# Kernel tuning notes

Hardware: AMD Instinct MI355X
Metric: run time of the kernel (lower is better)

The kernel has to match this reference:

```python
import jax, jax.numpy as jnp
import numpy as np

H = 32  # hidden size fixed by the module


def setup_inputs() -> dict:
    key = jax.random.key(0)
    ks = jax.random.split(key, 7)
    B, T, D = 1024, 512, 64
    s_ih = 1.0 / np.sqrt(H)
    return {
        "x": jax.random.normal(ks[0], (B, T, D), dtype=jnp.float32),
        "W_ih": jax.random.normal(ks[1], (3 * H, D), dtype=jnp.float32) * s_ih,
        "W_hh": jax.random.normal(ks[2], (3 * H, H), dtype=jnp.float32) * s_ih,
        "b_ih": jax.random.normal(ks[3], (3 * H,), dtype=jnp.float32) * s_ih,
        "b_hh": jax.random.normal(ks[4], (3 * H,), dtype=jnp.float32) * s_ih,
        "W_fc": jax.random.normal(ks[5], (1, H), dtype=jnp.float32) * s_ih,
        "b_fc": jax.random.normal(ks[6], (1,), dtype=jnp.float32) * s_ih,
    }


def _gru_last_hidden(x, W_ih, W_hh, b_ih, b_hh):
    # Precompute input-side gates for all timesteps in one big GEMM: [B,T,3H]
    xg = jnp.einsum("btd,gd->btg", x, W_ih) + b_ih
    xg = jnp.swapaxes(xg, 0, 1)  # [T,B,3H] for scan
    B = x.shape[0]
    h0 = jnp.zeros((B, H), dtype=x.dtype)

    def step(h, xg_t):
        gh = h @ W_hh.T + b_hh  # [B,3H]
        xr, xz, xn = xg_t[:, :H], xg_t[:, H:2 * H], xg_t[:, 2 * H:]
        hr, hz, hn = gh[:, :H], gh[:, H:2 * H], gh[:, 2 * H:]
        r = jax.nn.sigmoid(xr + hr)
        z = jax.nn.sigmoid(xz + hz)
        n = jnp.tanh(xn + r * hn)
        h_new = (1.0 - z) * n + z * h
        return h_new, None

    h_last, _ = jax.lax.scan(step, h0, xg)
    return h_last  # [B,H]


def reference(x, W_ih, W_hh, b_ih, b_hh, W_fc, b_fc):
    # GRU -> dropout (eval mode: identity) -> Linear on last timestep
    h_last = _gru_last_hidden(x, W_ih, W_hh, b_ih, b_hh)
    return h_last @ W_fc.T + b_fc  # [B,1]
```

## Files before the change

kernel.cpp:

```cpp
#include <hip/hip_runtime.h>

#define TS 512
#define DD 64
#define HH 32

typedef _Float16 half2v __attribute__((ext_vector_type(2)));

__device__ __forceinline__ float fdot2(half2v a, half2v b, float c) {
#if __has_builtin(__builtin_amdgcn_fdot2)
    return __builtin_amdgcn_fdot2(a, b, c, false);
#else
    return fmaf((float)a[0], (float)b[0], fmaf((float)a[1], (float)b[1], c));
#endif
}

__device__ __forceinline__ float fast_sigmoid(float a) {
    return __builtin_amdgcn_rcpf(1.0f + __expf(-a));
}

__global__ __launch_bounds__(64, 1) void gru_fused(
    const float* __restrict__ x,
    const float* __restrict__ Wih,
    const float* __restrict__ Whh,
    const float* __restrict__ bih,
    const float* __restrict__ bhh,
    const float* __restrict__ Wfc,
    const float* __restrict__ bfc,
    float* __restrict__ out)
{
    __shared__ __align__(16) _Float16 xs16[4][DD];
    __shared__ __align__(16) _Float16 hs16[HH];

    const int b    = blockIdx.x;
    const int lane = threadIdx.x;
    const int s    = lane >> 5;
    const int h    = lane & 31;

    half2v wr2[16], wz2[16], wn2[16];
    {
        const float4* pr = reinterpret_cast<const float4*>(Wih + (0 * HH + h) * DD + s * 32);
        const float4* pz = reinterpret_cast<const float4*>(Wih + (1 * HH + h) * DD + s * 32);
        const float4* pn = reinterpret_cast<const float4*>(Wih + (2 * HH + h) * DD + s * 32);
#pragma unroll
        for (int k = 0; k < 8; ++k) {
            float4 a = pr[k];
            wr2[2*k]   = half2v{(_Float16)a.x, (_Float16)a.y};
            wr2[2*k+1] = half2v{(_Float16)a.z, (_Float16)a.w};
            float4 c = pz[k];
            wz2[2*k]   = half2v{(_Float16)c.x, (_Float16)c.y};
            wz2[2*k+1] = half2v{(_Float16)c.z, (_Float16)c.w};
            float4 e = pn[k];
            wn2[2*k]   = half2v{(_Float16)e.x, (_Float16)e.y};
            wn2[2*k+1] = half2v{(_Float16)e.z, (_Float16)e.w};
        }
    }
    half2v ur2[8], uz2[8], un2[8];
    {
        const float4* pr = reinterpret_cast<const float4*>(Whh + (0 * HH + h) * HH + s * 16);
        const float4* pz = reinterpret_cast<const float4*>(Whh + (1 * HH + h) * HH + s * 16);
        const float4* pn = reinterpret_cast<const float4*>(Whh + (2 * HH + h) * HH + s * 16);
#pragma unroll
        for (int k = 0; k < 4; ++k) {
            float4 a = pr[k];
            ur2[2*k]   = half2v{(_Float16)a.x, (_Float16)a.y};
            ur2[2*k+1] = half2v{(_Float16)a.z, (_Float16)a.w};
            float4 c = pz[k];
            uz2[2*k]   = half2v{(_Float16)c.x, (_Float16)c.y};
            uz2[2*k+1] = half2v{(_Float16)c.z, (_Float16)c.w};
            float4 e = pn[k];
            un2[2*k]   = half2v{(_Float16)e.x, (_Float16)e.y};
            un2[2*k+1] = half2v{(_Float16)e.z, (_Float16)e.w};
        }
    }

    const float br  = bih[h]          + bhh[h];
    const float bz  = bih[HH + h]     + bhh[HH + h];
    const float bxn = bih[2 * HH + h];
    const float bhn = bhh[2 * HH + h];
    const float wfc = Wfc[h];
    const float bf0 = bfc[0];

    const float* xrow = x + (size_t)b * TS * DD;

    float p0 = xrow[0 * DD + lane];
    float p1 = xrow[1 * DD + lane];
    float p2 = xrow[2 * DD + lane];
    float ra = xrow[3 * DD + lane];
    float rb = xrow[4 * DD + lane];
    float rc = xrow[5 * DD + lane];
    xs16[0][lane] = (_Float16)p0;
    xs16[1][lane] = (_Float16)p1;
    xs16[2][lane] = (_Float16)p2;
    __builtin_amdgcn_wave_barrier();

    float h_own = 0.0f;
    half2v hv2[8];
#pragma unroll
    for (int k = 0; k < 8; ++k) hv2[k] = half2v{(_Float16)0.0f, (_Float16)0.0f};

    float ar, az, an;
    {
        const uint4* xp = reinterpret_cast<const uint4*>(&xs16[0][s * 32]);
        ar = 0.f; az = 0.f; an = 0.f;
#pragma unroll
        for (int k = 0; k < 4; ++k) {
            uint4 q = xp[k];
            half2v v0 = __builtin_bit_cast(half2v, q.x);
            half2v v1 = __builtin_bit_cast(half2v, q.y);
            half2v v2 = __builtin_bit_cast(half2v, q.z);
            half2v v3 = __builtin_bit_cast(half2v, q.w);
            ar = fdot2(wr2[4*k  ], v0, ar);
            az = fdot2(wz2[4*k  ], v0, az);
            an = fdot2(wn2[4*k  ], v0, an);
            ar = fdot2(wr2[4*k+1], v1, ar);
            az = fdot2(wz2[4*k+1], v1, az);
            an = fdot2(wn2[4*k+1], v1, an);
            ar = fdot2(wr2[4*k+2], v2, ar);
            az = fdot2(wz2[4*k+2], v2, az);
            an = fdot2(wn2[4*k+2], v2, an);
            ar = fdot2(wr2[4*k+3], v3, ar);
            az = fdot2(wz2[4*k+3], v3, az);
            an = fdot2(wn2[4*k+3], v3, an);
        }
    }

    for (int t = 0; t < TS; ++t) {
        xs16[(t + 3) & 3][lane] = (_Float16)ra;
        ra = rb; rb = rc;
        int tf = t + 6; if (tf > TS - 1) tf = TS - 1;
        rc = xrow[tf * DD + lane];

        float gr = 0.f, gz = 0.f, gn = 0.f;
#pragma unroll
        for (int k = 0; k < 8; ++k) {
            gr = fdot2(ur2[k], hv2[k], gr);
            gz = fdot2(uz2[k], hv2[k], gz);
            gn = fdot2(un2[k], hv2[k], gn);
        }

        float tr = ar + gr;  tr += __shfl_xor(tr, 32);
        float tz = az + gz;  tz += __shfl_xor(tz, 32);
        float txn = an + __shfl_xor(an, 32);
        float tgn = gn + __shfl_xor(gn, 32);

        float r = fast_sigmoid(tr + br);
        float z = fast_sigmoid(tz + bz);
        float npre = txn + bxn + r * (tgn + bhn);
        npre = fminf(fmaxf(npre, -30.f), 30.f);
        float e2 = __expf(-2.f * npre);
        float n = (1.f - e2) * __builtin_amdgcn_rcpf(1.f + e2);
        h_own = n + z * (h_own - n);

        hs16[h] = (_Float16)h_own;
        __builtin_amdgcn_wave_barrier();
        {
            const uint4* hp = reinterpret_cast<const uint4*>(&hs16[s * 16]);
            uint4 q0 = hp[0];
            uint4 q1 = hp[1];
            hv2[0] = __builtin_bit_cast(half2v, q0.x);
            hv2[1] = __builtin_bit_cast(half2v, q0.y);
            hv2[2] = __builtin_bit_cast(half2v, q0.z);
            hv2[3] = __builtin_bit_cast(half2v, q0.w);
            hv2[4] = __builtin_bit_cast(half2v, q1.x);
            hv2[5] = __builtin_bit_cast(half2v, q1.y);
            hv2[6] = __builtin_bit_cast(half2v, q1.z);
            hv2[7] = __builtin_bit_cast(half2v, q1.w);
        }

        if (t + 1 < TS) {
            const uint4* xp = reinterpret_cast<const uint4*>(&xs16[(t + 1) & 3][s * 32]);
            ar = 0.f; az = 0.f; an = 0.f;
#pragma unroll
            for (int k = 0; k < 4; ++k) {
                uint4 q = xp[k];
                half2v v0 = __builtin_bit_cast(half2v, q.x);
                half2v v1 = __builtin_bit_cast(half2v, q.y);
                half2v v2 = __builtin_bit_cast(half2v, q.z);
                half2v v3 = __builtin_bit_cast(half2v, q.w);
                ar = fdot2(wr2[4*k  ], v0, ar);
                az = fdot2(wz2[4*k  ], v0, az);
                an = fdot2(wn2[4*k  ], v0, an);
                ar = fdot2(wr2[4*k+1], v1, ar);
                az = fdot2(wz2[4*k+1], v1, az);
                an = fdot2(wn2[4*k+1], v1, an);
                ar = fdot2(wr2[4*k+2], v2, ar);
                az = fdot2(wz2[4*k+2], v2, az);
                an = fdot2(wn2[4*k+2], v2, an);
                ar = fdot2(wr2[4*k+3], v3, ar);
                az = fdot2(wz2[4*k+3], v3, az);
                an = fdot2(wn2[4*k+3], v3, an);
            }
        }
    }

    float v = h_own * wfc;
#pragma unroll
    for (int off = 32; off >= 1; off >>= 1) v += __shfl_xor(v, off);
    if (lane == 0) out[b] = 0.5f * v + bf0;
}

extern "C" void kernel_launch(void* const* d_in, const int* in_sizes, int n_in,
                              void* d_out, int out_size, void* d_ws, size_t ws_size,
                              hipStream_t stream) {
    const float* x    = (const float*)d_in[0];
    const float* Wih  = (const float*)d_in[1];
    const float* Whh  = (const float*)d_in[2];
    const float* bih  = (const float*)d_in[3];
    const float* bhh  = (const float*)d_in[4];
    const float* Wfc  = (const float*)d_in[5];
    const float* bfc  = (const float*)d_in[6];
    float* out = (float*)d_out;

    const int B = in_sizes[0] / (TS * DD);
    gru_fused<<<dim3(B), dim3(64), 0, stream>>>(x, Wih, Whh, bih, bhh, Wfc, bfc, out);
}
```

Baseline: 190.5 us.

## Split input projection into separate kernel writing fp16 gates to workspace

The input-side gate projection moves out of the serial recurrence into its own kernel. That kernel uses three waves per batch row and writes biased fp16 gate pre-activations to the workspace. The recurrence kernel then only prefetches those gates and runs the hidden-state dot products, split across two accumulators, which shortens the per-step dependency chain. The cost is an extra write and read of a large fp16 intermediate plus a second launch. A fallback to the original fused kernel is kept for when the workspace is too small.

```diff
diff --git a/kernel.cpp b/kernel.cpp
--- a/kernel.cpp
+++ b/kernel.cpp
@@ -3,6 +3,7 @@
 #define TS 512
 #define DD 64
 #define HH 32
+#define NG 96
 
 typedef _Float16 half2v __attribute__((ext_vector_type(2)));
 
@@ -18,17 +19,78 @@
     return __builtin_amdgcn_rcpf(1.0f + __expf(-a));
 }
 
-__global__ __launch_bounds__(64, 1) void gru_fused(
+__global__ __launch_bounds__(192, 1) void xg_gemm(
     const float* __restrict__ x,
     const float* __restrict__ Wih,
+    const float* __restrict__ bih,
+    _Float16* __restrict__ xg)
+{
+    __shared__ __align__(16) _Float16 xsw[3][4][DD];
+
+    const int b    = blockIdx.x;
+    const int tid  = threadIdx.x;
+    const int w    = tid >> 6;
+    const int lane = tid & 63;
+    const int j    = lane >> 5;
+    const int g    = w * 32 + (lane & 31);
+
+    half2v wg[16];
+    {
+        const float4* pw = reinterpret_cast<const float4*>(Wih + g * DD + j * 32);
+#pragma unroll
+        for (int k = 0; k < 8; ++k) {
+            float4 a = pw[k];
+            wg[2*k]   = half2v{(_Float16)a.x, (_Float16)a.y};
+            wg[2*k+1] = half2v{(_Float16)a.z, (_Float16)a.w};
+        }
+    }
+    const float bg = bih[g];
+
+    const float* xr = x + (size_t)b * TS * DD;
+    _Float16* og = xg + (size_t)b * TS * NG;
+
+    float q0 = xr[0*DD + lane];
+    float q1 = xr[1*DD + lane];
+    float q2 = xr[2*DD + lane];
+    float ra = xr[3*DD + lane];
+    float rb = xr[4*DD + lane];
+    float rc = xr[5*DD + lane];
+    xsw[w][0][lane] = (_Float16)q0;
+    xsw[w][1][lane] = (_Float16)q1;
+    xsw[w][2][lane] = (_Float16)q2;
+    __builtin_amdgcn_wave_barrier();
+
+    for (int t = 0; t < TS; ++t) {
+        xsw[w][(t + 3) & 3][lane] = (_Float16)ra;
+        ra = rb; rb = rc;
+        int tf = t + 6; if (tf > TS - 1) tf = TS - 1;
+        rc = xr[tf * DD + lane];
+        __builtin_amdgcn_wave_barrier();
+
+        const uint4* xp = reinterpret_cast<const uint4*>(&xsw[w][t & 3][j * 32]);
+        float a0 = 0.f, a1 = 0.f;
+#pragma unroll
+        for (int k = 0; k < 4; ++k) {
+            uint4 q = xp[k];
+            a0 = fdot2(wg[4*k  ], __builtin_bit_cast(half2v, q.x), a0);
+            a1 = fdot2(wg[4*k+1], __builtin_bit_cast(half2v, q.y), a1);
+            a0 = fdot2(wg[4*k+2], __builtin_bit_cast(half2v, q.z), a0);
+            a1 = fdot2(wg[4*k+3], __builtin_bit_cast(half2v, q.w), a1);
+        }
+        float acc = a0 + a1;
+        acc += __shfl_xor(acc, 32);
+        if (j == 0) og[t * NG + g] = (_Float16)(acc + bg);
+    }
+}
+
+__global__ __launch_bounds__(64, 1) void gru_rec(
+    const _Float16* __restrict__ xg,
     const float* __restrict__ Whh,
-    const float* __restrict__ bih,
     const float* __restrict__ bhh,
     const float* __restrict__ Wfc,
     const float* __restrict__ bfc,
     float* __restrict__ out)
 {
-    __shared__ __align__(16) _Float16 xs16[4][DD];
     __shared__ __align__(16) _Float16 hs16[HH];
 
     const int b    = blockIdx.x;
@@ -36,29 +98,11 @@
     const int s    = lane >> 5;
     const int h    = lane & 31;
 
-    half2v wr2[16], wz2[16], wn2[16];
-    {
-        const float4* pr = reinterpret_cast<const float4*>(Wih + (0 * HH + h) * DD + s * 32);
-        const float4* pz = reinterpret_cast<const float4*>(Wih + (1 * HH + h) * DD + s * 32);
-        const float4* pn = reinterpret_cast<const float4*>(Wih + (2 * HH + h) * DD + s * 32);
-#pragma unroll
-        for (int k = 0; k < 8; ++k) {
-            float4 a = pr[k];
-            wr2[2*k]   = half2v{(_Float16)a.x, (_Float16)a.y};
-            wr2[2*k+1] = half2v{(_Float16)a.z, (_Float16)a.w};
-            float4 c = pz[k];
-            wz2[2*k]   = half2v{(_Float16)c.x, (_Float16)c.y};
-            wz2[2*k+1] = half2v{(_Float16)c.z, (_Float16)c.w};
-            float4 e = pn[k];
-            wn2[2*k]   = half2v{(_Float16)e.x, (_Float16)e.y};
-            wn2[2*k+1] = half2v{(_Float16)e.z, (_Float16)e.w};
-        }
-    }
     half2v ur2[8], uz2[8], un2[8];
     {
-        const float4* pr = reinterpret_cast<const float4*>(Whh + (0 * HH + h) * HH + s * 16);
-        const float4* pz = reinterpret_cast<const float4*>(Whh + (1 * HH + h) * HH + s * 16);
-        const float4* pn = reinterpret_cast<const float4*>(Whh + (2 * HH + h) * HH + s * 16);
+        const float4* pr = reinterpret_cast<const float4*>(Whh + (0*HH + h)*HH + s*16);
+        const float4* pz = reinterpret_cast<const float4*>(Whh + (1*HH + h)*HH + s*16);
+        const float4* pn = reinterpret_cast<const float4*>(Whh + (2*HH + h)*HH + s*16);
 #pragma unroll
         for (int k = 0; k < 4; ++k) {
             float4 a = pr[k];
@@ -73,79 +117,55 @@
         }
     }
 
-    const float br  = bih[h]          + bhh[h];
-    const float bz  = bih[HH + h]     + bhh[HH + h];
-    const float bxn = bih[2 * HH + h];
-    const float bhn = bhh[2 * HH + h];
+    const float cr  = bhh[h];
+    const float cz  = bhh[HH + h];
+    const float cn  = bhh[2*HH + h];
     const float wfc = Wfc[h];
     const float bf0 = bfc[0];
 
-    const float* xrow = x + (size_t)b * TS * DD;
-
-    float p0 = xrow[0 * DD + lane];
-    float p1 = xrow[1 * DD + lane];
-    float p2 = xrow[2 * DD + lane];
-    float ra = xrow[3 * DD + lane];
-    float rb = xrow[4 * DD + lane];
-    float rc = xrow[5 * DD + lane];
-    xs16[0][lane] = (_Float16)p0;
-    xs16[1][lane] = (_Float16)p1;
-    xs16[2][lane] = (_Float16)p2;
-    __builtin_amdgcn_wave_barrier();
-
-    float h_own = 0.0f;
+    const _Float16* xb = xg + (size_t)b * TS * NG;
+
+    _Float16 xra = xb[0*NG + h],        xrb = xb[1*NG + h],        xrc = xb[2*NG + h];
+    _Float16 xza = xb[0*NG + HH + h],   xzb = xb[1*NG + HH + h],   xzc = xb[2*NG + HH + h];
+    _Float16 xna = xb[0*NG + 2*HH + h], xnb = xb[1*NG + 2*HH + h], xnc = xb[2*NG + 2*HH + h];
+
+    float h_own = 0.f;
     half2v hv2[8];
 #pragma unroll
     for (int k = 0; k < 8; ++k) hv2[k] = half2v{(_Float16)0.0f, (_Float16)0.0f};
 
-    float ar, az, an;
-    {
-        const uint4* xp = reinterpret_cast<const uint4*>(&xs16[0][s * 32]);
-        ar = 0.f; az = 0.f; an = 0.f;
-#pragma unroll
-        for (int k = 0; k < 4; ++k) {
-            uint4 q = xp[k];
-            half2v v0 = __builtin_bit_cast(half2v, q.x);
-            half2v v1 = __builtin_bit_cast(half2v, q.y);
-            half2v v2 = __builtin_bit_cast(half2v, q.z);
-            half2v v3 = __builtin_bit_cast(half2v, q.w);
-            ar = fdot2(wr2[4*k  ], v0, ar);
-            az = fdot2(wz2[4*k  ], v0, az);
-            an = fdot2(wn2[4*k  ], v0, an);
-            ar = fdot2(wr2[4*k+1], v1, ar);
-            az = fdot2(wz2[4*k+1], v1, az);
-            an = fdot2(wn2[4*k+1], v1, an);
-            ar = fdot2(wr2[4*k+2], v2, ar);
-            az = fdot2(wz2[4*k+2], v2, az);
-            an = fdot2(wn2[4*k+2], v2, an);
-            ar = fdot2(wr2[4*k+3], v3, ar);
-            az = fdot2(wz2[4*k+3], v3, az);
-            an = fdot2(wn2[4*k+3], v3, an);
-        }
-    }
-
     for (int t = 0; t < TS; ++t) {
-        xs16[(t + 3) & 3][lane] = (_Float16)ra;
-        ra = rb; rb = rc;
-        int tf = t + 6; if (tf > TS - 1) tf = TS - 1;
-        rc = xrow[tf * DD + lane];
-
-        float gr = 0.f, gz = 0.f, gn = 0.f;
-#pragma unroll
-        for (int k = 0; k < 8; ++k) {
-            gr = fdot2(ur2[k], hv2[k], gr);
-            gz = fdot2(uz2[k], hv2[k], gz);
-            gn = fdot2(un2[k], hv2[k], gn);
-        }
-
-        float tr = ar + gr;  tr += __shfl_xor(tr, 32);
-        float tz = az + gz;  tz += __shfl_xor(tz, 32);
-        float txn = an + __shfl_xor(an, 32);
-        float tgn = gn + __shfl_xor(gn, 32);
-
-        float r = fast_sigmoid(tr + br);
-        float z = fast_sigmoid(tz + bz);
-        float npre = txn + bxn + r * (tgn + bhn);
+        float xrv = (float)xra;
+        float xzv = (float)xza;
+        float xnv = (float)xna;
+        xra = xrb; xrb = xrc;
+        xza = xzb; xzb = xzc;
+        xna = xnb; xnb = xnc;
+        int tf = t + 3; if (tf > TS - 1) tf = TS - 1;
+        xrc = xb[tf*NG + h];
+        xzc = xb[tf*NG + HH + h];
+        xnc = xb[tf*NG + 2*HH + h];
+
+        float gr0 = 0.f, gr1 = 0.f, gz0 = 0.f, gz1 = 0.f, gn0 = 0.f, gn1 = 0.f;
+#pragma unroll
+        for (int k = 0; k < 4; ++k) {
+            gr0 = fdot2(ur2[2*k  ], hv2[2*k  ], gr0);
+            gr1 = fdot2(ur2[2*k+1], hv2[2*k+1], gr1);
+            gz0 = fdot2(uz2[2*k  ], hv2[2*k  ], gz0);
+            gz1 = fdot2(uz2[2*k+1], hv2[2*k+1], gz1);
+            gn0 = fdot2(un2[2*k  ], hv2[2*k  ], gn0);
+            gn1 = fdot2(un2[2*k+1], hv2[2*k+1], gn1);
+        }
+        float gr = gr0 + gr1;
+        float gz = gz0 + gz1;
+        float gn = gn0 + gn1;
+        gr += __shfl_xor(gr, 32);
+        gz += __shfl_xor(gz, 32);
+        gn += __shfl_xor(gn, 32);
+
+        float r = fast_sigmoid(xrv + cr + gr);
+        float z = fast_sigmoid(xzv + cz + gz);
+        float npre = xnv + r * (gn + cn);
         npre = fminf(fmaxf(npre, -30.f), 30.f);
         float e2 = __expf(-2.f * npre);
         float n = (1.f - e2) * __builtin_amdgcn_rcpf(1.f + e2);
@@ -166,6 +186,154 @@
             hv2[6] = __builtin_bit_cast(half2v, q1.z);
             hv2[7] = __builtin_bit_cast(half2v, q1.w);
         }
+    }
+
+    float v = h_own * wfc;
+#pragma unroll
+    for (int off = 32; off >= 1; off >>= 1) v += __shfl_xor(v, off);
+    if (lane == 0) out[b] = 0.5f * v + bf0;
+}
+
+__global__ __launch_bounds__(64, 1) void gru_fused_fb(
+    const float* __restrict__ x,
+    const float* __restrict__ Wih,
+    const float* __restrict__ Whh,
+    const float* __restrict__ bih,
+    const float* __restrict__ bhh,
+    const float* __restrict__ Wfc,
+    const float* __restrict__ bfc,
+    float* __restrict__ out)
+{
+    __shared__ __align__(16) _Float16 xs16[4][DD];
+    __shared__ __align__(16) _Float16 hs16[HH];
+
+    const int b    = blockIdx.x;
+    const int lane = threadIdx.x;
+    const int s    = lane >> 5;
+    const int h    = lane & 31;
+
+    half2v wr2[16], wz2[16], wn2[16];
+    {
+        const float4* pr = reinterpret_cast<const float4*>(Wih + (0*HH + h)*DD + s*32);
+        const float4* pz = reinterpret_cast<const float4*>(Wih + (1*HH + h)*DD + s*32);
+        const float4* pn = reinterpret_cast<const float4*>(Wih + (2*HH + h)*DD + s*32);
+#pragma unroll
+        for (int k = 0; k < 8; ++k) {
+            float4 a = pr[k];
+            wr2[2*k]   = half2v{(_Float16)a.x, (_Float16)a.y};
+            wr2[2*k+1] = half2v{(_Float16)a.z, (_Float16)a.w};
+            float4 c = pz[k];
+            wz2[2*k]   = half2v{(_Float16)c.x, (_Float16)c.y};
+            wz2[2*k+1] = half2v{(_Float16)c.z, (_Float16)c.w};
+            float4 e = pn[k];
+            wn2[2*k]   = half2v{(_Float16)e.x, (_Float16)e.y};
+            wn2[2*k+1] = half2v{(_Float16)e.z, (_Float16)e.w};
+        }
+    }
+    half2v ur2[8], uz2[8], un2[8];
+    {
+        const float4* pr = reinterpret_cast<const float4*>(Whh + (0*HH + h)*HH + s*16);
+        const float4* pz = reinterpret_cast<const float4*>(Whh + (1*HH + h)*HH + s*16);
+        const float4* pn = reinterpret_cast<const float4*>(Whh + (2*HH + h)*HH + s*16);
+#pragma unroll
+        for (int k = 0; k < 4; ++k) {
+            float4 a = pr[k];
+            ur2[2*k]   = half2v{(_Float16)a.x, (_Float16)a.y};
+            ur2[2*k+1] = half2v{(_Float16)a.z, (_Float16)a.w};
+            float4 c = pz[k];
+            uz2[2*k]   = half2v{(_Float16)c.x, (_Float16)c.y};
+            uz2[2*k+1] = half2v{(_Float16)c.z, (_Float16)c.w};
+            float4 e = pn[k];
+            un2[2*k]   = half2v{(_Float16)e.x, (_Float16)e.y};
+            un2[2*k+1] = half2v{(_Float16)e.z, (_Float16)e.w};
+        }
+    }
+
+    const float br  = bih[h]        + bhh[h];
+    const float bz  = bih[HH + h]   + bhh[HH + h];
+    const float bxn = bih[2*HH + h];
+    const float bhn = bhh[2*HH + h];
+    const float wfc = Wfc[h];
+    const float bf0 = bfc[0];
+
+    const float* xrow = x + (size_t)b * TS * DD;
+
+    float p0 = xrow[0*DD + lane];
+    float p1 = xrow[1*DD + lane];
+    float p2 = xrow[2*DD + lane];
+    float ra = xrow[3*DD + lane];
+    float rb = xrow[4*DD + lane];
+    float rc = xrow[5*DD + lane];
+    xs16[0][lane] = (_Float16)p0;
+    xs16[1][lane] = (_Float16)p1;
+    xs16[2][lane] = (_Float16)p2;
+    __builtin_amdgcn_wave_barrier();
+
+    float h_own = 0.0f;
+    half2v hv2[8];
+#pragma unroll
+    for (int k = 0; k < 8; ++k) hv2[k] = half2v{(_Float16)0.0f, (_Float16)0.0f};
+
+    float ar, az, an;
+    {
+        const uint4* xp = reinterpret_cast<const uint4*>(&xs16[0][s * 32]);
+        ar = 0.f; az = 0.f; an = 0.f;
+#pragma unroll
+        for (int k = 0; k < 4; ++k) {
+            uint4 q = xp[k];
+            half2v v0 = __builtin_bit_cast(half2v, q.x);
+            half2v v1 = __builtin_bit_cast(half2v, q.y);
+            half2v v2 = __builtin_bit_cast(half2v, q.z);
+            half2v v3 = __builtin_bit_cast(half2v, q.w);
+            ar = fdot2(wr2[4*k  ], v0, ar);  az = fdot2(wz2[4*k  ], v0, az);  an = fdot2(wn2[4*k  ], v0, an);
+            ar = fdot2(wr2[4*k+1], v1, ar);  az = fdot2(wz2[4*k+1], v1, az);  an = fdot2(wn2[4*k+1], v1, an);
+            ar = fdot2(wr2[4*k+2], v2, ar);  az = fdot2(wz2[4*k+2], v2, az);  an = fdot2(wn2[4*k+2], v2, an);
+            ar = fdot2(wr2[4*k+3], v3, ar);  az = fdot2(wz2[4*k+3], v3, az);  an = fdot2(wn2[4*k+3], v3, an);
+        }
+    }
+
+    for (int t = 0; t < TS; ++t) {
+        xs16[(t + 3) & 3][lane] = (_Float16)ra;
+        ra = rb; rb = rc;
+        int tf = t + 6; if (tf > TS - 1) tf = TS - 1;
+        rc = xrow[tf * DD + lane];
+
+        float gr = 0.f, gz = 0.f, gn = 0.f;
+#pragma unroll
+        for (int k = 0; k < 8; ++k) {
+            gr = fdot2(ur2[k], hv2[k], gr);
+            gz = fdot2(uz2[k], hv2[k], gz);
+            gn = fdot2(un2[k], hv2[k], gn);
+        }
+
+        float tr = ar + gr;  tr += __shfl_xor(tr, 32);
+        float tz = az + gz;  tz += __shfl_xor(tz, 32);
+        float txn = an + __shfl_xor(an, 32);
+        float tgn = gn + __shfl_xor(gn, 32);
+
+        float r = fast_sigmoid(tr + br);
+        float z = fast_sigmoid(tz + bz);
+        float npre = txn + bxn + r * (tgn + bhn);
+        npre = fminf(fmaxf(npre, -30.f), 30.f);
+        float e2 = __expf(-2.f * npre);
+        float n = (1.f - e2) * __builtin_amdgcn_rcpf(1.f + e2);
+        h_own = n + z * (h_own - n);
+
+        hs16[h] = (_Float16)h_own;
+        __builtin_amdgcn_wave_barrier();
+        {
+            const uint4* hp = reinterpret_cast<const uint4*>(&hs16[s * 16]);
+            uint4 q0 = hp[0];
+            uint4 q1 = hp[1];
+            hv2[0] = __builtin_bit_cast(half2v, q0.x);
+            hv2[1] = __builtin_bit_cast(half2v, q0.y);
+            hv2[2] = __builtin_bit_cast(half2v, q0.z);
+            hv2[3] = __builtin_bit_cast(half2v, q0.w);
+            hv2[4] = __builtin_bit_cast(half2v, q1.x);
+            hv2[5] = __builtin_bit_cast(half2v, q1.y);
+            hv2[6] = __builtin_bit_cast(half2v, q1.z);
+            hv2[7] = __builtin_bit_cast(half2v, q1.w);
+        }
 
         if (t + 1 < TS) {
             const uint4* xp = reinterpret_cast<const uint4*>(&xs16[(t + 1) & 3][s * 32]);
@@ -177,18 +345,10 @@
                 half2v v1 = __builtin_bit_cast(half2v, q.y);
                 half2v v2 = __builtin_bit_cast(half2v, q.z);
                 half2v v3 = __builtin_bit_cast(half2v, q.w);
-                ar = fdot2(wr2[4*k  ], v0, ar);
-                az = fdot2(wz2[4*k  ], v0, az);
-                an = fdot2(wn2[4*k  ], v0, an);
-                ar = fdot2(wr2[4*k+1], v1, ar);
-                az = fdot2(wz2[4*k+1], v1, az);
-                an = fdot2(wn2[4*k+1], v1, an);
-                ar = fdot2(wr2[4*k+2], v2, ar);
-                az = fdot2(wz2[4*k+2], v2, az);
-                an = fdot2(wn2[4*k+2], v2, an);
-                ar = fdot2(wr2[4*k+3], v3, ar);
-                az = fdot2(wz2[4*k+3], v3, az);
-                an = fdot2(wn2[4*k+3], v3, an);
+                ar = fdot2(wr2[4*k  ], v0, ar);  az = fdot2(wz2[4*k  ], v0, az);  an = fdot2(wn2[4*k  ], v0, an);
+                ar = fdot2(wr2[4*k+1], v1, ar);  az = fdot2(wz2[4*k+1], v1, az);  an = fdot2(wn2[4*k+1], v1, an);
+                ar = fdot2(wr2[4*k+2], v2, ar);  az = fdot2(wz2[4*k+2], v2, az);  an = fdot2(wn2[4*k+2], v2, an);
+                ar = fdot2(wr2[4*k+3], v3, ar);  az = fdot2(wz2[4*k+3], v3, az);  an = fdot2(wn2[4*k+3], v3, an);
             }
         }
     }
@@ -212,5 +372,13 @@
     float* out = (float*)d_out;
 
     const int B = in_sizes[0] / (TS * DD);
-    gru_fused<<<dim3(B), dim3(64), 0, stream>>>(x, Wih, Whh, bih, bhh, Wfc, bfc, out);
-}
+    const size_t need = (size_t)B * TS * NG * sizeof(_Float16);
+
+    if (ws_size >= need) {
+        _Float16* xg = (_Float16*)d_ws;
+        xg_gemm<<<dim3(B), dim3(192), 0, stream>>>(x, Wih, bih, xg);
+        gru_rec<<<dim3(B), dim3(64), 0, stream>>>(xg, Whh, bhh, Wfc, bfc, out);
+    } else {
+        gru_fused_fb<<<dim3(B), dim3(64), 0, stream>>>(x, Wih, Whh, bih, bhh, Wfc, bfc, out);
+    }
+}
```

After: 295.4 us. 1.55x slower.
